# Optimization experiments

Hardware: AMD Instinct MI355X
Metric: run time of the kernel (lower is better)

The kernel has to match this reference:

```python
import jax, jax.numpy as jnp
import numpy as np

N = 50000      # nodes
E = 800000     # edges (avg degree 16)
DIN = 128      # input_dim
H = 256        # hidden_channels
DOUT = 64      # output_dim


def _glorot(k, shape):
    lim = float(np.sqrt(6.0 / (shape[0] + shape[1])))
    return jax.random.uniform(k, shape, jnp.float32, -lim, lim)


def setup_inputs() -> dict:
    key = jax.random.key(0)
    ks = jax.random.split(key, 10)
    return {
        "x": jax.random.normal(ks[0], (N, DIN), jnp.float32),
        "W1": _glorot(ks[3], (DIN, H)), "b1": jnp.zeros((H,), jnp.float32),
        "W2": _glorot(ks[4], (H, H)),   "b2": jnp.zeros((H,), jnp.float32),
        "L1w": _glorot(ks[5], (H, DIN)), "L1b": jnp.zeros((DIN,), jnp.float32),
        "L2w": _glorot(ks[6], (DIN, H)), "L2b": jnp.zeros((H,), jnp.float32),
        "W3": _glorot(ks[7], (H, DOUT)), "b3": jnp.zeros((DOUT,), jnp.float32),
        "adj": jax.random.randint(ks[1], (2, E), 0, N),
        "adj2": jax.random.randint(ks[2], (2, E), 0, N),
        "mode": 1,  # 1 -> 'l' (return logits); 0 -> softmax over classes
    }


def gcn_conv(x, edge_index, W, b):
    """PyG-style GCNConv: add self-loops, symmetric D^-1/2 A D^-1/2 norm,
    aggregate neighbor features, then (here fused) linear transform."""
    n = x.shape[0]
    loop = jnp.arange(n)
    src = jnp.concatenate([edge_index[0], loop])  # message sources (j)
    dst = jnp.concatenate([edge_index[1], loop])  # aggregation targets (i)
    deg = jax.ops.segment_sum(jnp.ones(src.shape[0], x.dtype), dst, num_segments=n)
    dinv = jax.lax.rsqrt(jnp.maximum(deg, 1.0))   # deg >= 1 due to self-loops
    norm = dinv[src] * dinv[dst]                  # [E+N]
    h = x @ W                                     # transform first (smaller of the two dims either way)
    msg = h[src] * norm[:, None]                  # gather + scale, [E+N, out]
    return jax.ops.segment_sum(msg, dst, num_segments=n) + b


def reference(x, W1, b1, W2, b2, L1w, L1b, L2w, L2b, W3, b3, adj, adj2, mode):
    h = jax.nn.relu(gcn_conv(x, adj, W1, b1))      # GCNConv(in->h) on adj
    h = jax.nn.relu(gcn_conv(h, adj2, W2, b2))     # GCNConv(h->h) on adj2
    h = jax.nn.relu(h @ L1w + L1b)                 # Linear(h->in)
    h = jax.nn.relu(h @ L2w + L2b)                 # Linear(in->h)
    out = gcn_conv(h, adj2, W3, b3)                # GCNConv(h->out) on adj2
    # dropout has p=0 -> identity
    return out if mode == 1 else jax.nn.softmax(out, axis=1)
```

## Files before the change

kernel.cpp:

```cpp
#include <hip/hip_runtime.h>
#include <hip/hip_bf16.h>
#include <cstdint>
#include <cstddef>

#define NNODES 50000
#define NEDGES 800000
#define D_IN   128
#define D_H    256
#define D_OUT  64
#define BSH    9
#define BKN    (1 << BSH)
#define NBKT   ((NNODES + BKN - 1) / BKN)
#define MAXB   12288
#define CHUNK  2048
#define QMAX   32639.0f

typedef __attribute__((ext_vector_type(8))) short bf16x8;
typedef __attribute__((ext_vector_type(4))) float f32x4;
typedef __attribute__((ext_vector_type(4))) int   i32x4;

__device__ __forceinline__ unsigned short f2bf(float f) {
    unsigned u = __builtin_bit_cast(unsigned, f);
    unsigned r = (u + 0x7FFFu + ((u >> 16) & 1u)) >> 16;
    return (unsigned short)r;
}
__device__ __forceinline__ float bf2f(unsigned short h) {
    unsigned u = ((unsigned)h) << 16;
    return __builtin_bit_cast(float, u);
}


__global__ __launch_bounds__(256) void k_bin(const int* __restrict__ adjA, const int* __restrict__ adjB,
                                             int* __restrict__ bcnt, unsigned* __restrict__ binned, int e) {
    __shared__ int h[NBKT], pfx[NBKT], put[NBKT], gbase[NBKT];
    __shared__ unsigned stage[CHUNK];
    const int g = blockIdx.y;
    const int* srcp = g ? adjB : adjA;
    const int* dstp = srcp + e;
    unsigned* outp = binned + (size_t)g * NBKT * MAXB;
    int* bc = bcnt + g * NBKT;
    const int tid = threadIdx.x;
    const int base = blockIdx.x * CHUNK;
    const int nrem = min(CHUNK, e - base);
    if (nrem <= 0) return;

    for (int t = tid; t < NBKT; t += 256) { h[t] = 0; put[t] = 0; }
    __syncthreads();

    unsigned pv[8];
    int bv[8];
    #pragma unroll
    for (int q = 0; q < 8; ++q) {
        int i = base + q * 256 + tid;
        bv[q] = -1;
        if (i < e) {
            int s = srcp[i];
            int d = dstp[i];
            pv[q] = ((unsigned)d << 16) | (unsigned)s;
            bv[q] = d >> BSH;
            atomicAdd(&h[bv[q]], 1);
        }
    }
    __syncthreads();
    if (tid == 0) {
        int r = 0;
        for (int k = 0; k < NBKT; ++k) { pfx[k] = r; r += h[k]; }
    }
    __syncthreads();
    #pragma unroll
    for (int q = 0; q < 8; ++q) {
        if (bv[q] >= 0) {
            int p = pfx[bv[q]] + atomicAdd(&put[bv[q]], 1);
            stage[p] = pv[q];
        }
    }
    __syncthreads();
    if (tid < NBKT && h[tid] > 0) gbase[tid] = atomicAdd(&bc[tid], h[tid]);
    __syncthreads();
    for (int idx = tid; idx < nrem; idx += 256) {
        unsigned v = stage[idx];
        int bb = v >> (16 + BSH);
        outp[(size_t)bb * MAXB + gbase[bb] + (idx - pfx[bb])] = v;
    }
}

__global__ void k_bktscan(const int* __restrict__ bcnt, int* __restrict__ bbase,
                          int* __restrict__ rp1, int* __restrict__ rp2) {
    __shared__ int s[2][NBKT];
    int t = threadIdx.x;
    if (t < NBKT) s[0][t] = bcnt[t];
    else if (t < 2 * NBKT) s[1][t - NBKT] = bcnt[t];
    __syncthreads();
    if (t < 2) {
        int r = 0;
        for (int k = 0; k < NBKT; ++k) { int v = s[t][k]; s[t][k] = r; r += v; }
    }
    __syncthreads();
    if (t < NBKT) bbase[t] = s[0][t];
    else if (t < 2 * NBKT) bbase[t] = s[1][t - NBKT];
    if (t == 0) { rp1[NNODES] = NEDGES; rp2[NNODES] = NEDGES; }
}

__global__ __launch_bounds__(256) void k_csr_bucket(const unsigned* __restrict__ binned,
                                                    const int* __restrict__ bcnt, const int* __restrict__ bbase,
                                                    int* __restrict__ rp1, int* __restrict__ rp2,
                                                    float* __restrict__ dinv1, float* __restrict__ dinv2,
                                                    int* __restrict__ col1, int* __restrict__ col2, int n) {
    __shared__ int lc[BKN];
    __shared__ int loff[BKN];
    __shared__ int ps[256];
    __shared__ int srt[MAXB];
    const int g = blockIdx.y;
    const int b = blockIdx.x;
    const unsigned* in = binned + (size_t)g * NBKT * MAXB + (size_t)b * MAXB;
    int* rp = g ? rp2 : rp1;
    float* dinv = g ? dinv2 : dinv1;
    int* col = g ? col2 : col1;
    const int nb = bcnt[g * NBKT + b];
    const int base0 = bbase[g * NBKT + b];
    const int nodebase = b << BSH;
    const int tid = threadIdx.x;

    for (int t = tid; t < BKN; t += 256) lc[t] = 0;
    __syncthreads();
    for (int t = tid; t < nb; t += 256)
        atomicAdd(&lc[(in[t] >> 16) & (BKN - 1)], 1);
    __syncthreads();
    int c0 = lc[2 * tid], c1 = lc[2 * tid + 1];
    int pair = c0 + c1;
    int sum = pair;
    ps[tid] = pair;
    __syncthreads();
    #pragma unroll
    for (int off = 1; off < 256; off <<= 1) {
        int u = (tid >= off) ? ps[tid - off] : 0;
        __syncthreads();
        sum += u;
        ps[tid] = sum;
        __syncthreads();
    }
    int excl = sum - pair;
    loff[2 * tid] = excl;
    loff[2 * tid + 1] = excl + c0;
    __syncthreads();
    for (int t = tid; t < BKN; t += 256) {
        int node = nodebase + t;
        if (node < n) {
            rp[node] = base0 + loff[t];
            dinv[node] = rsqrtf((float)(lc[t] + 1));
        }
    }
    __syncthreads();
    for (int t = tid; t < nb; t += 256) {
        unsigned v = in[t];
        int pos = atomicAdd(&loff[(v >> 16) & (BKN - 1)], 1);
        srt[pos] = (int)(v & 0xFFFFu);
    }
    __syncthreads();
    for (int t = tid; t < nb; t += 256) col[base0 + t] = srt[t];
}


template<int F, bool PRESCALE>
__global__ __launch_bounds__(256) void k_quant(const float* __restrict__ in, const float* __restrict__ dscale,
                                               short* __restrict__ q, float* __restrict__ qs, int n) {
    constexpr int VPT = F / 64;
    const int lane = threadIdx.x & 63;
    const int i = blockIdx.x * 4 + (threadIdx.x >> 6);
    if (i >= n) return;
    float v[VPT];
    const float* p = in + (size_t)i * F + lane * VPT;
    if constexpr (VPT == 4) { float4 t = *(const float4*)p; v[0] = t.x; v[1] = t.y; v[2] = t.z; v[3] = t.w; }
    else if constexpr (VPT == 2) { float2 t = *(const float2*)p; v[0] = t.x; v[1] = t.y; }
    else v[0] = *p;
    if constexpr (PRESCALE) {
        float d = dscale[i];
        #pragma unroll
        for (int c = 0; c < VPT; ++c) v[c] *= d;
    }
    float m = 0.f;
    #pragma unroll
    for (int c = 0; c < VPT; ++c) m = fmaxf(m, fabsf(v[c]));
    #pragma unroll
    for (int off = 32; off > 0; off >>= 1) m = fmaxf(m, __shfl_xor(m, off));
    float inv = (m > 0.f) ? 32767.0f / m : 0.f;
    short* qp = q + (size_t)i * F + lane * VPT;
    if constexpr (VPT == 4) {
        short4 o;
        o.x = (short)__float2int_rn(v[0] * inv);
        o.y = (short)__float2int_rn(v[1] * inv);
        o.z = (short)__float2int_rn(v[2] * inv);
        o.w = (short)__float2int_rn(v[3] * inv);
        *(short4*)qp = o;
    } else if constexpr (VPT == 2) {
        short2 o;
        o.x = (short)__float2int_rn(v[0] * inv);
        o.y = (short)__float2int_rn(v[1] * inv);
        *(short2*)qp = o;
    } else {
        *qp = (short)__float2int_rn(v[0] * inv);
    }
    if (lane == 0) qs[i] = m * (1.0f / 32767.0f);
}


template<int F, int OUTM>
__global__ __launch_bounds__(256) void k_agg3(const short* __restrict__ q, const float* __restrict__ qs,
                                              const int* __restrict__ rp, const int* __restrict__ col,
                                              const float* __restrict__ dinv, const float* __restrict__ bias,
                                              void* __restrict__ outv, float* __restrict__ qs_out, int n) {
    constexpr int VPT = F / 64;
    const int lane = threadIdx.x & 63;
    const int i = blockIdx.x * 4 + (threadIdx.x >> 6);
    if (i >= n) return;
    const short* ql = q + lane * VPT;
    float acc[VPT];
    #pragma unroll
    for (int c = 0; c < VPT; ++c) acc[c] = 0.f;

    int k = rp[i], end = rp[i + 1];

    auto body1 = [&](int j) {
        float s = qs[j];
        const short* pj = ql + (size_t)j * F;
        if constexpr (VPT == 4) {
            short4 v = *(const short4*)pj;
            acc[0] += s * (float)v.x; acc[1] += s * (float)v.y;
            acc[2] += s * (float)v.z; acc[3] += s * (float)v.w;
        } else if constexpr (VPT == 2) {
            short2 v = *(const short2*)pj;
            acc[0] += s * (float)v.x; acc[1] += s * (float)v.y;
        } else {
            acc[0] += s * (float)(*pj);
        }
    };

    body1(i);
    for (; k + 4 <= end; k += 4) {
        int j0 = col[k], j1 = col[k + 1], j2 = col[k + 2], j3 = col[k + 3];
        float s0 = qs[j0], s1 = qs[j1], s2 = qs[j2], s3 = qs[j3];
        if constexpr (VPT == 4) {
            short4 v0 = *(const short4*)(ql + (size_t)j0 * F);
            short4 v1 = *(const short4*)(ql + (size_t)j1 * F);
            short4 v2 = *(const short4*)(ql + (size_t)j2 * F);
            short4 v3 = *(const short4*)(ql + (size_t)j3 * F);
            acc[0] += s0 * (float)v0.x + s1 * (float)v1.x + s2 * (float)v2.x + s3 * (float)v3.x;
            acc[1] += s0 * (float)v0.y + s1 * (float)v1.y + s2 * (float)v2.y + s3 * (float)v3.y;
            acc[2] += s0 * (float)v0.z + s1 * (float)v1.z + s2 * (float)v2.z + s3 * (float)v3.z;
            acc[3] += s0 * (float)v0.w + s1 * (float)v1.w + s2 * (float)v2.w + s3 * (float)v3.w;
        } else if constexpr (VPT == 2) {
            short2 v0 = *(const short2*)(ql + (size_t)j0 * F);
            short2 v1 = *(const short2*)(ql + (size_t)j1 * F);
            short2 v2 = *(const short2*)(ql + (size_t)j2 * F);
            short2 v3 = *(const short2*)(ql + (size_t)j3 * F);
            acc[0] += s0 * (float)v0.x + s1 * (float)v1.x + s2 * (float)v2.x + s3 * (float)v3.x;
            acc[1] += s0 * (float)v0.y + s1 * (float)v1.y + s2 * (float)v2.y + s3 * (float)v3.y;
        } else {
            float v0 = (float)ql[(size_t)j0 * F];
            float v1 = (float)ql[(size_t)j1 * F];
            float v2 = (float)ql[(size_t)j2 * F];
            float v3 = (float)ql[(size_t)j3 * F];
            acc[0] += s0 * v0 + s1 * v1 + s2 * v2 + s3 * v3;
        }
    }
    for (; k < end; ++k) body1(col[k]);

    float di = dinv[i];
    if constexpr (OUTM == 0) {
        float vals[VPT];
        float m = 0.f;
        #pragma unroll
        for (int c = 0; c < VPT; ++c) { vals[c] = acc[c] * di; m = fmaxf(m, fabsf(vals[c])); }
        #pragma unroll
        for (int off = 32; off > 0; off >>= 1) m = fmaxf(m, __shfl_xor(m, off));
        float inv = (m > 0.f) ? QMAX / m : 0.f;
        unsigned ph = 0, pl = 0;
        #pragma unroll
        for (int c = 0; c < VPT; ++c) {
            int qv = __float2int_rn(vals[c] * inv);
            int ah = (qv + 128) >> 8;
            int al = qv - (ah << 8);
            ph |= (unsigned)(ah & 0xFF) << (8 * c);
            pl |= (unsigned)(al & 0xFF) << (8 * c);
        }
        unsigned char* o8h = (unsigned char*)outv;
        unsigned char* o8l = o8h + (size_t)n * F;
        if constexpr (VPT == 4) {
            *(unsigned*)(o8h + (size_t)i * F + lane * 4) = ph;
            *(unsigned*)(o8l + (size_t)i * F + lane * 4) = pl;
        } else if constexpr (VPT == 2) {
            *(unsigned short*)(o8h + (size_t)i * F + lane * 2) = (unsigned short)ph;
            *(unsigned short*)(o8l + (size_t)i * F + lane * 2) = (unsigned short)pl;
        } else {
            o8h[(size_t)i * F + lane] = (unsigned char)ph;
            o8l[(size_t)i * F + lane] = (unsigned char)pl;
        }
        if (lane == 0) qs_out[i] = m * (1.0f / QMAX);
    } else {
        float* o = (float*)outv + (size_t)i * F + lane * VPT;
        #pragma unroll
        for (int c = 0; c < VPT; ++c) o[c] = acc[c] * di + bias[lane * VPT + c];
    }
}


__device__ __forceinline__ void wconv1(const float* __restrict__ W, unsigned short* __restrict__ Th,
                                       unsigned short* __restrict__ Tl, int idx, int K, int Nc) {
    int k = idx / Nc, n = idx - k * Nc;
    float v = W[idx];
    unsigned short h = f2bf(v);
    unsigned short l = f2bf(v - bf2f(h));
    Th[(size_t)n * K + k] = h;
    Tl[(size_t)n * K + k] = l;
}

__global__ void k_wconv_all(const float* L1w, const float* L2w, const float* W3,
                            unsigned short* L1h, unsigned short* L1l, unsigned short* L2h, unsigned short* L2l,
                            unsigned short* W3h, unsigned short* W3l) {
    int idx = blockIdx.x * blockDim.x + threadIdx.x;
    if (idx < 32768)        wconv1(L1w, L1h, L1l, idx, D_H, D_IN);
    else if (idx < 65536)   wconv1(L2w, L2h, L2l, idx - 32768, D_IN, D_H);
    else if (idx < 81920)   wconv1(W3, W3h, W3l, idx - 65536, D_H, D_OUT);
}


__global__ __launch_bounds__(256) void k_wconv_i8(const float* __restrict__ W1, const float* __restrict__ W2,
        signed char* __restrict__ B1h, signed char* __restrict__ B1l,
        signed char* __restrict__ B2h, signed char* __restrict__ B2l,
        float* __restrict__ ws1, float* __restrict__ ws2) {
    const int c4 = blockIdx.x * 4 + (threadIdx.x >> 6);
    const int lane = threadIdx.x & 63;
    const float* W; signed char *Bh, *Bl; float* ws; int K, c;
    if (c4 < 256) { W = W1; Bh = B1h; Bl = B1l; ws = ws1; K = D_IN; c = c4; }
    else          { W = W2; Bh = B2h; Bl = B2l; ws = ws2; K = D_H;  c = c4 - 256; }
    float m = 0.f;
    for (int k = lane; k < K; k += 64) m = fmaxf(m, fabsf(W[(size_t)k * D_H + c]));
    #pragma unroll
    for (int off = 32; off > 0; off >>= 1) m = fmaxf(m, __shfl_xor(m, off));
    float inv = (m > 0.f) ? QMAX / m : 0.f;
    for (int k = lane; k < K; k += 64) {
        int qv = __float2int_rn(W[(size_t)k * D_H + c] * inv);
        int ah = (qv + 128) >> 8;
        int al = qv - (ah << 8);
        Bh[(size_t)c * K + k] = (signed char)ah;
        Bl[(size_t)c * K + k] = (signed char)al;
    }
    if (lane == 0) ws[c] = m * (1.0f / QMAX);
}


template<bool RELU, bool BIAS, int OUTM>
__global__ __launch_bounds__(256) void k_gemm_i8(const unsigned char* __restrict__ A8,
        const float* __restrict__ qsr,
        const signed char* __restrict__ B8h, const signed char* __restrict__ B8l,
        const float* __restrict__ wsc,
        const float* __restrict__ bias, const float* __restrict__ dscale,
        void* __restrict__ Cv, int M, int K, int Nc, int ncb) {
    constexpr int PADB = 68;
    __shared__ unsigned char As_h[128][PADB];
    __shared__ unsigned char As_l[128][PADB];
    __shared__ unsigned char Bs_h[64][PADB];
    __shared__ unsigned char Bs_l[64][PADB];

    const int nwg = gridDim.x;
    const int b = blockIdx.x;
    const int q8 = nwg >> 3, r8 = nwg & 7;
    const int xcd = b & 7;
    const int swz = (xcd < r8 ? xcd * (q8 + 1) : r8 * (q8 + 1) + (xcd - r8) * q8) + (b >> 3);
    const int row0 = (swz / ncb) * 128;
    const int col0 = (swz % ncb) * 64;

    const int tid = threadIdx.x;
    const int lane = tid & 63;
    const int wv = tid >> 6;

    i32x4 acc_hh[2][4], acc_mm[2][4], acc_ll[2][4];
    #pragma unroll
    for (int m = 0; m < 2; ++m)
        #pragma unroll
        for (int n = 0; n < 4; ++n) {
            acc_hh[m][n] = (i32x4)(0);
            acc_mm[m][n] = (i32x4)(0);
            acc_ll[m][n] = (i32x4)(0);
        }

    const int srow = tid >> 1;
    const int skh = (tid & 1) * 32;
    int arow = row0 + srow;
    if (arow >= M) arow = M - 1;
    const unsigned char* aph = A8 + (size_t)arow * K + skh;
    const unsigned char* apl = aph + (size_t)M * K;

    const int bn = tid >> 2;
    const int bko = (tid & 3) * 16;
    const signed char* bph = B8h + (size_t)(col0 + bn) * K + bko;
    const signed char* bpl = B8l + (size_t)(col0 + bn) * K + bko;

    const int fr = lane & 15;
    const int fko = (lane >> 4) * 16;

    const int nk = K >> 6;
    for (int kt = 0; kt < nk; ++kt) {
        uint4 ah0 = *(const uint4*)(aph + kt * 64);
        uint4 ah1 = *(const uint4*)(aph + kt * 64 + 16);
        uint4 al0 = *(const uint4*)(apl + kt * 64);
        uint4 al1 = *(const uint4*)(apl + kt * 64 + 16);
        uint4 bh0 = *(const uint4*)(bph + kt * 64);
        uint4 bl0 = *(const uint4*)(bpl + kt * 64);

        __syncthreads();

        *(uint4*)&As_h[srow][skh] = ah0;
        *(uint4*)&As_h[srow][skh + 16] = ah1;
        *(uint4*)&As_l[srow][skh] = al0;
        *(uint4*)&As_l[srow][skh + 16] = al1;
        *(uint4*)&Bs_h[bn][bko] = bh0;
        *(uint4*)&Bs_l[bn][bko] = bl0;

        __syncthreads();

        i32x4 fah[2], fal[2], fbh[4], fbl[4];
        #pragma unroll
        for (int m = 0; m < 2; ++m) {
            fah[m] = *(const i32x4*)&As_h[wv * 32 + m * 16 + fr][fko];
            fal[m] = *(const i32x4*)&As_l[wv * 32 + m * 16 + fr][fko];
        }
        #pragma unroll
        for (int n = 0; n < 4; ++n) {
            fbh[n] = *(const i32x4*)&Bs_h[n * 16 + fr][fko];
            fbl[n] = *(const i32x4*)&Bs_l[n * 16 + fr][fko];
        }
        #pragma unroll
        for (int m = 0; m < 2; ++m)
            #pragma unroll
            for (int n = 0; n < 4; ++n) {
                acc_hh[m][n] = __builtin_amdgcn_mfma_i32_16x16x64_i8(fah[m], fbh[n], acc_hh[m][n], 0, 0, 0);
                acc_mm[m][n] = __builtin_amdgcn_mfma_i32_16x16x64_i8(fah[m], fbl[n], acc_mm[m][n], 0, 0, 0);
                acc_mm[m][n] = __builtin_amdgcn_mfma_i32_16x16x64_i8(fal[m], fbh[n], acc_mm[m][n], 0, 0, 0);
                acc_ll[m][n] = __builtin_amdgcn_mfma_i32_16x16x64_i8(fal[m], fbl[n], acc_ll[m][n], 0, 0, 0);
            }
    }

    float bv[4], wv_[4];
    #pragma unroll
    for (int n = 0; n < 4; ++n) {
        const int c = col0 + n * 16 + fr;
        bv[n] = BIAS ? bias[c] : 0.f;
        wv_[n] = wsc[c];
    }
    const int rbase = row0 + wv * 32 + (lane >> 4) * 4;
    #pragma unroll
    for (int m = 0; m < 2; ++m) {
        #pragma unroll
        for (int j = 0; j < 4; ++j) {
            const int r = rbase + m * 16 + j;
            if (r >= M) continue;
            const float qr = qsr[r];
            float ds = 1.f;
            if constexpr (OUTM == 1) ds = dscale[r];
            #pragma unroll
            for (int n = 0; n < 4; ++n) {
                const int c = col0 + n * 16 + fr;
                float dot = 65536.f * (float)acc_hh[m][n][j] + 256.f * (float)acc_mm[m][n][j]
                          + (float)acc_ll[m][n][j];
                float o = dot * qr * wv_[n] + bv[n];
                if constexpr (RELU) o = fmaxf(o, 0.f);
                if constexpr (OUTM == 1) {
                    ((float*)Cv)[(size_t)r * Nc + c] = o * ds;
                } else {
                    unsigned short h = f2bf(o);
                    unsigned short l = f2bf(o - bf2f(h));
                    unsigned short* C2 = (unsigned short*)Cv + (size_t)r * 2 * Nc + c;
                    C2[0] = h;
                    C2[Nc] = l;
                }
            }
        }
    }
}


template<bool RELU, bool BIAS, int OUTM>
__global__ __launch_bounds__(256) void k_gemm3(const unsigned short* __restrict__ Ahl,
        const unsigned short* __restrict__ Bth, const unsigned short* __restrict__ Btl,
        const float* __restrict__ bias, const float* __restrict__ dscale,
        void* __restrict__ Cv, int M, int K, int Nc, int ncb) {
    constexpr int PAD = 66;
    __shared__ unsigned short As_h[128][PAD];
    __shared__ unsigned short As_l[128][PAD];
    __shared__ unsigned short Bs_h[64][PAD];
    __shared__ unsigned short Bs_l[64][PAD];

    const int nwg = gridDim.x;
    const int b = blockIdx.x;
    const int q8 = nwg >> 3, r8 = nwg & 7;
    const int xcd = b & 7;
    const int swz = (xcd < r8 ? xcd * (q8 + 1) : r8 * (q8 + 1) + (xcd - r8) * q8) + (b >> 3);
    const int row0 = (swz / ncb) * 128;
    const int col0 = (swz % ncb) * 64;

    const int tid = threadIdx.x;
    const int lane = tid & 63;
    const int wv = tid >> 6;

    f32x4 acc[2][4];
    #pragma unroll
    for (int m = 0; m < 2; ++m)
        #pragma unroll
        for (int n = 0; n < 4; ++n) acc[m][n] = (f32x4)(0.f);

    const int srow = tid >> 1;
    const int skh = (tid & 1) * 32;
    int arow = row0 + srow;
    if (arow >= M) arow = M - 1;
    const unsigned short* aph = Ahl + (size_t)arow * 2 * K + skh;
    const unsigned short* apl = aph + K;

    const int bn = tid >> 2;
    const int bko = (tid & 3) * 16;
    const unsigned short* bph = Bth + (size_t)(col0 + bn) * K + bko;
    const unsigned short* bpl = Btl + (size_t)(col0 + bn) * K + bko;

    const int fr = lane & 15;
    const int fk = (lane >> 4) * 8;

    const int nk = K >> 6;
    for (int kt = 0; kt < nk; ++kt) {
        uint4 ah0 = *(const uint4*)(aph + kt * 64);
        uint4 ah1 = *(const uint4*)(aph + kt * 64 + 8);
        uint4 ah2 = *(const uint4*)(aph + kt * 64 + 16);
        uint4 ah3 = *(const uint4*)(aph + kt * 64 + 24);
        uint4 al0 = *(const uint4*)(apl + kt * 64);
        uint4 al1 = *(const uint4*)(apl + kt * 64 + 8);
        uint4 al2 = *(const uint4*)(apl + kt * 64 + 16);
        uint4 al3 = *(const uint4*)(apl + kt * 64 + 24);
        uint4 bh0 = *(const uint4*)(bph + kt * 64);
        uint4 bh1 = *(const uint4*)(bph + kt * 64 + 8);
        uint4 bl0 = *(const uint4*)(bpl + kt * 64);
        uint4 bl1 = *(const uint4*)(bpl + kt * 64 + 8);

        __syncthreads();

        *(uint4*)&As_h[srow][skh] = ah0;
        *(uint4*)&As_h[srow][skh + 8] = ah1;
        *(uint4*)&As_h[srow][skh + 16] = ah2;
        *(uint4*)&As_h[srow][skh + 24] = ah3;
        *(uint4*)&As_l[srow][skh] = al0;
        *(uint4*)&As_l[srow][skh + 8] = al1;
        *(uint4*)&As_l[srow][skh + 16] = al2;
        *(uint4*)&As_l[srow][skh + 24] = al3;
        *(uint4*)&Bs_h[bn][bko] = bh0;
        *(uint4*)&Bs_h[bn][bko + 8] = bh1;
        *(uint4*)&Bs_l[bn][bko] = bl0;
        *(uint4*)&Bs_l[bn][bko + 8] = bl1;

        __syncthreads();

        #pragma unroll
        for (int ks = 0; ks < 2; ++ks) {
            const int ko = ks * 32 + fk;
            bf16x8 ah[2], al[2], bh[4], bl[4];
            #pragma unroll
            for (int m = 0; m < 2; ++m) {
                ah[m] = *(const bf16x8*)&As_h[wv * 32 + m * 16 + fr][ko];
                al[m] = *(const bf16x8*)&As_l[wv * 32 + m * 16 + fr][ko];
            }
            #pragma unroll
            for (int n = 0; n < 4; ++n) {
                bh[n] = *(const bf16x8*)&Bs_h[n * 16 + fr][ko];
                bl[n] = *(const bf16x8*)&Bs_l[n * 16 + fr][ko];
            }
            #pragma unroll
            for (int m = 0; m < 2; ++m)
                #pragma unroll
                for (int n = 0; n < 4; ++n) {
                    acc[m][n] = __builtin_amdgcn_mfma_f32_16x16x32_bf16(ah[m], bh[n], acc[m][n], 0, 0, 0);
                    acc[m][n] = __builtin_amdgcn_mfma_f32_16x16x32_bf16(ah[m], bl[n], acc[m][n], 0, 0, 0);
                    acc[m][n] = __builtin_amdgcn_mfma_f32_16x16x32_bf16(al[m], bh[n], acc[m][n], 0, 0, 0);
                }
        }
    }

    float bv[4];
    #pragma unroll
    for (int n = 0; n < 4; ++n) bv[n] = BIAS ? bias[col0 + n * 16 + fr] : 0.f;
    const int rbase = row0 + wv * 32 + (lane >> 4) * 4;
    #pragma unroll
    for (int m = 0; m < 2; ++m) {
        #pragma unroll
        for (int j = 0; j < 4; ++j) {
            const int r = rbase + m * 16 + j;
            if (r >= M) continue;
            float ds = 1.f;
            if constexpr (OUTM == 1) ds = dscale[r];
            #pragma unroll
            for (int n = 0; n < 4; ++n) {
                const int c = col0 + n * 16 + fr;
                float o = acc[m][n][j] + bv[n];
                if constexpr (RELU) o = fmaxf(o, 0.f);
                if constexpr (OUTM == 1) {
                    ((float*)Cv)[(size_t)r * Nc + c] = o * ds;
                } else {
                    unsigned short h = f2bf(o);
                    unsigned short l = f2bf(o - bf2f(h));
                    unsigned short* C2 = (unsigned short*)Cv + (size_t)r * 2 * Nc + c;
                    C2[0] = h;
                    C2[Nc] = l;
                }
            }
        }
    }
}


__global__ __launch_bounds__(256) void k_softmax(float* __restrict__ out, const int* __restrict__ mode, int n) {
    if (*mode == 1) return;
    int lane = threadIdx.x & 63;
    int i = blockIdx.x * 4 + (threadIdx.x >> 6);
    if (i >= n) return;
    float v = out[(size_t)i * 64 + lane];
    float m = v;
    #pragma unroll
    for (int off = 32; off > 0; off >>= 1) m = fmaxf(m, __shfl_xor(m, off));
    float e = __expf(v - m);
    float s = e;
    #pragma unroll
    for (int off = 32; off > 0; off >>= 1) s += __shfl_xor(s, off);
    out[(size_t)i * 64 + lane] = e / s;
}


extern "C" void kernel_launch(void* const* d_in, const int* in_sizes, int n_in,
                              void* d_out, int out_size, void* d_ws, size_t ws_size,
                              hipStream_t stream) {
    const float* x   = (const float*)d_in[0];
    const float* W1  = (const float*)d_in[1];
    const float* b1  = (const float*)d_in[2];
    const float* W2  = (const float*)d_in[3];
    const float* b2  = (const float*)d_in[4];
    const float* L1w = (const float*)d_in[5];
    const float* L1b = (const float*)d_in[6];
    const float* L2w = (const float*)d_in[7];
    const float* L2b = (const float*)d_in[8];
    const float* W3  = (const float*)d_in[9];
    const float* b3  = (const float*)d_in[10];
    const int* adj   = (const int*)d_in[11];
    const int* adj2  = (const int*)d_in[12];
    const int* mode  = (const int*)d_in[13];
    float* out = (float*)d_out;

    char* ws = (char*)d_ws;
    auto alloc = [&](size_t bytes) {
        char* p = ws;
        ws += (bytes + 255) & ~(size_t)255;
        return p;
    };
    char*  bufA  = alloc((size_t)NNODES * 256 * 4);
    char*  bufB  = alloc((size_t)NNODES * 256 * 4);
    int*   rp1   = (int*)alloc((NNODES + 1) * 4);
    int*   col1  = (int*)alloc((size_t)NEDGES * 4);
    int*   rp2   = (int*)alloc((NNODES + 1) * 4);
    int*   col2  = (int*)alloc((size_t)NEDGES * 4);
    float* dinv1 = (float*)alloc(NNODES * 4);
    float* dinv2 = (float*)alloc(NNODES * 4);
    int*   bcnt  = (int*)alloc(2 * NBKT * 4);
    int*   bbase = (int*)alloc(2 * NBKT * 4);
    float* qsA   = (float*)alloc(NNODES * 4);
    float* qsB   = (float*)alloc(NNODES * 4);
    signed char* B1h = (signed char*)alloc(256 * D_IN);
    signed char* B1l = (signed char*)alloc(256 * D_IN);
    signed char* B2h = (signed char*)alloc(256 * D_H);
    signed char* B2l = (signed char*)alloc(256 * D_H);
    float* ws1 = (float*)alloc(256 * 4);
    float* ws2 = (float*)alloc(256 * 4);
    unsigned short* L1h = (unsigned short*)alloc(D_H * D_IN * 2);
    unsigned short* L1l = (unsigned short*)alloc(D_H * D_IN * 2);
    unsigned short* L2h = (unsigned short*)alloc(D_IN * D_H * 2);
    unsigned short* L2l = (unsigned short*)alloc(D_IN * D_H * 2);
    unsigned short* W3h = (unsigned short*)alloc(D_H * D_OUT * 2);
    unsigned short* W3l = (unsigned short*)alloc(D_H * D_OUT * 2);
    unsigned* binned = (unsigned*)bufA;

    const int AGB = (NNODES + 3) / 4;
    const int MT = (NNODES + 127) / 128;
    const int BINB = (NEDGES + CHUNK - 1) / CHUNK;

    k_wconv_all<<<(81920 + 255) / 256, 256, 0, stream>>>(L1w, L2w, W3,
        L1h, L1l, L2h, L2l, W3h, W3l);
    k_wconv_i8<<<128, 256, 0, stream>>>(W1, W2, B1h, B1l, B2h, B2l, ws1, ws2);

    hipMemsetAsync(bcnt, 0, 2 * NBKT * 4, stream);
    k_bin<<<dim3(BINB, 2), 256, 0, stream>>>(adj, adj2, bcnt, binned, NEDGES);
    k_bktscan<<<1, 256, 0, stream>>>(bcnt, bbase, rp1, rp2);
    k_csr_bucket<<<dim3(NBKT, 2), 256, 0, stream>>>(binned, bcnt, bbase, rp1, rp2,
                                                    dinv1, dinv2, col1, col2, NNODES);

    k_quant<128, true><<<AGB, 256, 0, stream>>>(x, dinv1, (short*)bufA, qsA, NNODES);
    k_agg3<128, 0><<<AGB, 256, 0, stream>>>((const short*)bufA, qsA, rp1, col1, dinv1, nullptr, bufB, qsB, NNODES);
    k_gemm_i8<true, true, 1><<<MT * 4, 256, 0, stream>>>(
        (const unsigned char*)bufB, qsB, B1h, B1l, ws1, b1, dinv2, bufA, NNODES, D_IN, D_H, 4);
    k_quant<256, false><<<AGB, 256, 0, stream>>>((const float*)bufA, nullptr, (short*)bufB, qsA, NNODES);
    k_agg3<256, 0><<<AGB, 256, 0, stream>>>((const short*)bufB, qsA, rp2, col2, dinv2, nullptr, bufA, qsB, NNODES);
    k_gemm_i8<true, true, 2><<<MT * 4, 256, 0, stream>>>(
        (const unsigned char*)bufA, qsB, B2h, B2l, ws2, b2, nullptr, bufB, NNODES, D_H, D_H, 4);
    k_gemm3<true, true, 2><<<MT * 2, 256, 0, stream>>>(
        (const unsigned short*)bufB, L1h, L1l, L1b, nullptr, bufA, NNODES, D_H, D_IN, 2);
    k_gemm3<true, true, 2><<<MT * 4, 256, 0, stream>>>(
        (const unsigned short*)bufA, L2h, L2l, L2b, nullptr, bufB, NNODES, D_IN, D_H, 4);
    k_gemm3<false, false, 1><<<MT * 1, 256, 0, stream>>>(
        (const unsigned short*)bufB, W3h, W3l, nullptr, dinv2, bufA, NNODES, D_H, D_OUT, 1);
    k_quant<64, false><<<AGB, 256, 0, stream>>>((const float*)bufA, nullptr, (short*)bufB, qsA, NNODES);
    k_agg3<64, 1><<<AGB, 256, 0, stream>>>((const short*)bufB, qsA, rp2, col2, dinv2, b3, out, nullptr, NNODES);
    k_softmax<<<AGB, 256, 0, stream>>>(out, mode, NNODES);
}
```

Baseline: 353.8 us.

## Fuse W3 GEMM with int16 row quantization, drop low-low MFMA term, unroll gather by 8

```diff
diff --git a/kernel.cpp b/kernel.cpp
--- a/kernel.cpp
+++ b/kernel.cpp
@@ -236,6 +236,36 @@
     };
 
     body1(i);
+    if constexpr (VPT == 4) {
+        for (; k + 8 <= end; k += 8) {
+            int j[8]; float s[8]; short4 v[8];
+            #pragma unroll
+            for (int u = 0; u < 8; ++u) j[u] = col[k + u];
+            #pragma unroll
+            for (int u = 0; u < 8; ++u) s[u] = qs[j[u]];
+            #pragma unroll
+            for (int u = 0; u < 8; ++u) v[u] = *(const short4*)(ql + (size_t)j[u] * F);
+            #pragma unroll
+            for (int u = 0; u < 8; ++u) {
+                acc[0] += s[u] * (float)v[u].x; acc[1] += s[u] * (float)v[u].y;
+                acc[2] += s[u] * (float)v[u].z; acc[3] += s[u] * (float)v[u].w;
+            }
+        }
+    } else if constexpr (VPT == 2) {
+        for (; k + 8 <= end; k += 8) {
+            int j[8]; float s[8]; short2 v[8];
+            #pragma unroll
+            for (int u = 0; u < 8; ++u) j[u] = col[k + u];
+            #pragma unroll
+            for (int u = 0; u < 8; ++u) s[u] = qs[j[u]];
+            #pragma unroll
+            for (int u = 0; u < 8; ++u) v[u] = *(const short2*)(ql + (size_t)j[u] * F);
+            #pragma unroll
+            for (int u = 0; u < 8; ++u) {
+                acc[0] += s[u] * (float)v[u].x; acc[1] += s[u] * (float)v[u].y;
+            }
+        }
+    }
     for (; k + 4 <= end; k += 4) {
         int j0 = col[k], j1 = col[k + 1], j2 = col[k + 2], j3 = col[k + 3];
         float s0 = qs[j0], s1 = qs[j1], s2 = qs[j2], s3 = qs[j3];
@@ -374,14 +404,13 @@
     const int lane = tid & 63;
     const int wv = tid >> 6;
 
-    i32x4 acc_hh[2][4], acc_mm[2][4], acc_ll[2][4];
+    i32x4 acc_hh[2][4], acc_mm[2][4];
     #pragma unroll
     for (int m = 0; m < 2; ++m)
         #pragma unroll
         for (int n = 0; n < 4; ++n) {
             acc_hh[m][n] = (i32x4)(0);
             acc_mm[m][n] = (i32x4)(0);
-            acc_ll[m][n] = (i32x4)(0);
         }
 
     const int srow = tid >> 1;
@@ -437,7 +466,6 @@
                 acc_hh[m][n] = __builtin_amdgcn_mfma_i32_16x16x64_i8(fah[m], fbh[n], acc_hh[m][n], 0, 0, 0);
                 acc_mm[m][n] = __builtin_amdgcn_mfma_i32_16x16x64_i8(fah[m], fbl[n], acc_mm[m][n], 0, 0, 0);
                 acc_mm[m][n] = __builtin_amdgcn_mfma_i32_16x16x64_i8(fal[m], fbh[n], acc_mm[m][n], 0, 0, 0);
-                acc_ll[m][n] = __builtin_amdgcn_mfma_i32_16x16x64_i8(fal[m], fbl[n], acc_ll[m][n], 0, 0, 0);
             }
     }
 
@@ -461,8 +489,7 @@
             #pragma unroll
             for (int n = 0; n < 4; ++n) {
                 const int c = col0 + n * 16 + fr;
-                float dot = 65536.f * (float)acc_hh[m][n][j] + 256.f * (float)acc_mm[m][n][j]
-                          + (float)acc_ll[m][n][j];
+                float dot = 65536.f * (float)acc_hh[m][n][j] + 256.f * (float)acc_mm[m][n][j];
                 float o = dot * qr * wv_[n] + bv[n];
                 if constexpr (RELU) o = fmaxf(o, 0.f);
                 if constexpr (OUTM == 1) {
@@ -484,7 +511,7 @@
 __global__ __launch_bounds__(256) void k_gemm3(const unsigned short* __restrict__ Ahl,
         const unsigned short* __restrict__ Bth, const unsigned short* __restrict__ Btl,
         const float* __restrict__ bias, const float* __restrict__ dscale,
-        void* __restrict__ Cv, int M, int K, int Nc, int ncb) {
+        void* __restrict__ Cv, float* __restrict__ qs_out, int M, int K, int Nc, int ncb) {
     constexpr int PAD = 66;
     __shared__ unsigned short As_h[128][PAD];
     __shared__ unsigned short As_l[128][PAD];
@@ -581,10 +608,43 @@
         }
     }
 
+    const int rbase = row0 + wv * 32 + (lane >> 4) * 4;
+    if constexpr (OUTM == 3) {
+        #pragma unroll
+        for (int m = 0; m < 2; ++m) {
+            #pragma unroll
+            for (int j = 0; j < 4; ++j) {
+                const int r = rbase + m * 16 + j;
+                const int rr = (r < M) ? r : (M - 1);
+                const float ds = dscale[rr];
+                float vals[4];
+                float mx = 0.f;
+                #pragma unroll
+                for (int n = 0; n < 4; ++n) {
+                    float o = acc[m][n][j] * ds;
+                    vals[n] = o;
+                    mx = fmaxf(mx, fabsf(o));
+                }
+                mx = fmaxf(mx, __shfl_xor(mx, 1));
+                mx = fmaxf(mx, __shfl_xor(mx, 2));
+                mx = fmaxf(mx, __shfl_xor(mx, 4));
+                mx = fmaxf(mx, __shfl_xor(mx, 8));
+                float inv = (mx > 0.f) ? 32767.0f / mx : 0.f;
+                if (r < M) {
+                    short* C2 = (short*)Cv + (size_t)r * Nc;
+                    #pragma unroll
+                    for (int n = 0; n < 4; ++n)
+                        C2[n * 16 + fr] = (short)__float2int_rn(vals[n] * inv);
+                    if (fr == 0) qs_out[r] = mx * (1.0f / 32767.0f);
+                }
+            }
+        }
+        return;
+    }
+
     float bv[4];
     #pragma unroll
     for (int n = 0; n < 4; ++n) bv[n] = BIAS ? bias[col0 + n * 16 + fr] : 0.f;
-    const int rbase = row0 + wv * 32 + (lane >> 4) * 4;
     #pragma unroll
     for (int m = 0; m < 2; ++m) {
         #pragma unroll
@@ -704,12 +764,11 @@
     k_gemm_i8<true, true, 2><<<MT * 4, 256, 0, stream>>>(
         (const unsigned char*)bufA, qsB, B2h, B2l, ws2, b2, nullptr, bufB, NNODES, D_H, D_H, 4);
     k_gemm3<true, true, 2><<<MT * 2, 256, 0, stream>>>(
-        (const unsigned short*)bufB, L1h, L1l, L1b, nullptr, bufA, NNODES, D_H, D_IN, 2);
+        (const unsigned short*)bufB, L1h, L1l, L1b, nullptr, bufA, nullptr, NNODES, D_H, D_IN, 2);
     k_gemm3<true, true, 2><<<MT * 4, 256, 0, stream>>>(
-        (const unsigned short*)bufA, L2h, L2l, L2b, nullptr, bufB, NNODES, D_IN, D_H, 4);
-    k_gemm3<false, false, 1><<<MT * 1, 256, 0, stream>>>(
-        (const unsigned short*)bufB, W3h, W3l, nullptr, dinv2, bufA, NNODES, D_H, D_OUT, 1);
-    k_quant<64, false><<<AGB, 256, 0, stream>>>((const float*)bufA, nullptr, (short*)bufB, qsA, NNODES);
-    k_agg3<64, 1><<<AGB, 256, 0, stream>>>((const short*)bufB, qsA, rp2, col2, dinv2, b3, out, nullptr, NNODES);
+        (const unsigned short*)bufA, L2h, L2l, L2b, nullptr, bufB, nullptr, NNODES, D_IN, D_H, 4);
+    k_gemm3<false, false, 3><<<MT * 1, 256, 0, stream>>>(
+        (const unsigned short*)bufB, W3h, W3l, nullptr, dinv2, bufA, qsA, NNODES, D_H, D_OUT, 1);
+    k_agg3<64, 1><<<AGB, 256, 0, stream>>>((const short*)bufA, qsA, rp2, col2, dinv2, b3, out, nullptr, NNODES);
     k_softmax<<<AGB, 256, 0, stream>>>(out, mode, NNODES);
 }
```

New measurement: 326.3 us. 7.8% less time.
